# Kernel optimization log

Hardware: AMD Instinct MI355X
Metric: run time of the kernel (lower is better)

## Reference

```python
import jax, jax.numpy as jnp
import numpy as np

N = 100000      # nodes
E = 1600000     # edges (avg degree 16)
DIM = 128
HEADS = 8
HEAD_DIM = DIM // HEADS


def setup_inputs() -> dict:
    key = jax.random.key(0)
    k = jax.random.split(key, 6)
    stdv = 1.0 / np.sqrt(HEAD_DIM)  # init scale from reset_parameters
    x = jax.random.normal(k[0], (N, DIM), dtype=jnp.float32)
    edge_index = jax.random.randint(k[1], (2, E), 0, N, dtype=jnp.int32)
    W = jax.random.uniform(k[2], (DIM, DIM), jnp.float32, -stdv, stdv)
    b_proj = jnp.zeros((DIM,), jnp.float32)
    att_src = jax.random.uniform(k[3], (1, HEADS, HEAD_DIM), jnp.float32, -stdv, stdv)
    att_dst = jax.random.uniform(k[4], (1, HEADS, HEAD_DIM), jnp.float32, -stdv, stdv)
    bias = jnp.zeros((DIM,), jnp.float32)
    return {"x": x, "edge_index": edge_index, "W": W, "b_proj": b_proj,
            "att_src": att_src, "att_dst": att_dst, "bias": bias}


def reference(x, edge_index, W, b_proj, att_src, att_dst, bias):
    n = x.shape[0]
    # project, split heads: [N, H, Hd]
    xh = (x @ W.T + b_proj).reshape(n, HEADS, HEAD_DIM)
    # add_remaining_self_loops (random edges assumed loop-free)
    loops = jnp.arange(n, dtype=edge_index.dtype)
    src = jnp.concatenate([edge_index[0], loops])  # x_j index
    dst = jnp.concatenate([edge_index[1], loops])  # aggregation index
    # per-node attention logits [N, H]
    a_src = jnp.einsum('nhd,hd->nh', xh, att_src[0])
    a_dst = jnp.einsum('nhd,hd->nh', xh, att_dst[0])
    # per-edge score [Etot, H]
    alpha = jax.nn.leaky_relu(a_src[src] + a_dst[dst], negative_slope=0.2)
    # segment softmax over edges grouped by destination (self loops => no empty segments)
    mx = jax.ops.segment_max(alpha, dst, num_segments=n)
    ex = jnp.exp(alpha - mx[dst])
    denom = jax.ops.segment_sum(ex, dst, num_segments=n)
    alpha = ex / denom[dst]
    # message = alpha * x_j, scatter-add to destination
    msg = alpha[:, :, None] * xh[src]                      # [Etot, H, Hd]
    out = jax.ops.segment_sum(msg, dst, num_segments=n)    # [N, H, Hd]
    return out.reshape(n, DIM) + bias
```

## Files before the change

kernel.cpp:

```cpp
#include <hip/hip_runtime.h>
#include <hip/hip_bf16.h>

typedef __hip_bfloat16 bf16;
typedef __hip_bfloat162 bf162;
typedef __attribute__((ext_vector_type(8))) short short8;
typedef __attribute__((ext_vector_type(4))) float f32x4;

#define NN 100000
#define NE 1600000
#define ETOT (NE + NN)
#define DIM 128
#define HEADS 8

#define BSH 9
#define NBUK ((NN + 511) >> BSH)
#define EPB 2048
#define B1 ((ETOT + EPB - 1) / EPB)
#define MAXPER 40

__device__ __forceinline__ float lrelu(float v) { return v > 0.f ? v : 0.2f * v; }

__device__ __forceinline__ float load1(const void* p, int i, int isbf) {
    return isbf ? __bfloat162float(((const bf16*)p)[i]) : ((const float*)p)[i];
}
__device__ __forceinline__ float2 load2(const void* p, size_t pairIdx, int isbf) {
    if (isbf) return __bfloat1622float2(((const bf162*)p)[pairIdx]);
    return ((const float2*)p)[pairIdx];
}
__device__ __forceinline__ short f2bf(float f) {
    bf16 h = __float2bfloat16(f);
    return *reinterpret_cast<short*>(&h);
}

__global__ __launch_bounds__(256) void aug_kernel(
    const void* __restrict__ W, const void* __restrict__ bproj,
    const void* __restrict__ atts, const void* __restrict__ attd,
    int* __restrict__ flag, bf16* __restrict__ waug, float* __restrict__ wc)
{
    __shared__ bf16 Wl[128 * 128];
    __shared__ float av[256];
    __shared__ float red[256];
    const int tid = threadIdx.x;

    {
        const bf16* wb = (const bf16*)W;
        float m = 0.f;
        for (int i = tid; i < 8192; i += 256) {
            float v = fabsf(__bfloat162float(wb[i]));
            if (!(v < 1e30f)) v = 1e30f;
            m = fmaxf(m, v);
        }
        red[tid] = m;
        __syncthreads();
        for (int s = 128; s > 0; s >>= 1) {
            if (tid < s) red[tid] = fmaxf(red[tid], red[tid + s]);
            __syncthreads();
        }
    }
    const int isbf = (red[0] < 1.0f) ? 1 : 0;
    if (tid == 0) *flag = isbf;

    for (int i = tid; i < 2048; i += 256) {
        short8 v;
        if (isbf) {
            v = ((const short8*)W)[i];
        } else {
            const float* wp = (const float*)W + (size_t)i * 8;
            #pragma unroll
            for (int j = 0; j < 8; ++j) v[j] = f2bf(wp[j]);
        }
        ((short8*)Wl)[i] = v;
    }
    av[tid & 255] = (tid < 128) ? load1(atts, tid, isbf)
                                : load1(attd, tid - 128, isbf);
    __syncthreads();

    #pragma unroll
    for (int it = 0; it < 8; ++it) {
        const int o = tid + it * 256;
        const int row = o >> 7, col = o & 127;
        const int h = row & 7;
        const int ao = (row < 8) ? 0 : 128;
        float s = 0.f;
        #pragma unroll
        for (int t = 0; t < 16; ++t)
            s += av[ao + h * 16 + t] * __bfloat162float(Wl[(h * 16 + t) * 128 + col]);
        waug[o] = __float2bfloat16(s);
    }
    if (tid < 16) {
        const int h = tid & 7;
        const int ao = (tid < 8) ? 0 : 128;
        float s = 0.f;
        #pragma unroll
        for (int t = 0; t < 16; ++t)
            s += load1(bproj, h * 16 + t, isbf) * av[ao + h * 16 + t];
        wc[tid] = s;
    }
}

__global__ __launch_bounds__(256) void proj_mfma_kernel(
    const void* __restrict__ x, const void* __restrict__ W,
    const void* __restrict__ bproj, const bf16* __restrict__ waug,
    const float* __restrict__ wc, const int* __restrict__ flag,
    bf16* __restrict__ xh, float* __restrict__ asrc, float* __restrict__ adst)
{
    __shared__ short8 Wf[2304];
    __shared__ float bsh[DIM], csh[16];

    const int isbf = *flag;
    const int tid = threadIdx.x;

    for (int c = tid; c < 2048; c += 256) {
        int j = c >> 4, kc = c & 15;
        int kb = kc >> 2, quad = kc & 3;
        int lane = quad * 16 + (j & 15);
        int jt = j >> 4;
        short8 v;
        if (isbf) {
            v = ((const short8*)W)[c];
        } else {
            const float* wp = (const float*)W + (size_t)j * DIM + kc * 8;
            #pragma unroll
            for (int i = 0; i < 8; ++i) v[i] = f2bf(wp[i]);
        }
        Wf[(jt * 4 + kb) * 64 + lane] = v;
    }
    {
        int c = tid;
        if (c < 256) {
            int j2 = c >> 4, kc = c & 15;
            int kb = kc >> 2, quad = kc & 3;
            Wf[(32 + kb) * 64 + quad * 16 + j2] = ((const short8*)waug)[c];
        }
    }
    if (tid < DIM) bsh[tid] = load1(bproj, tid, isbf);
    if (tid < 16)  csh[tid] = wc[tid];
    __syncthreads();

    const int w = tid >> 6;
    const int l = tid & 63;
    const int quad = l >> 4, mr = l & 15;
    const int n0 = blockIdx.x * 64 + w * 16;
    const int nArd = min(n0 + mr, NN - 1);

    short8 afr[4];
    if (isbf) {
        const short8* xp = (const short8*)x + (size_t)nArd * 16;
        #pragma unroll
        for (int kb = 0; kb < 4; ++kb) afr[kb] = xp[kb * 4 + quad];
    } else {
        const float* xp = (const float*)x + (size_t)nArd * DIM;
        #pragma unroll
        for (int kb = 0; kb < 4; ++kb) {
            const float* cp = xp + kb * 32 + quad * 8;
            float4 c0 = *(const float4*)cp;
            float4 c1 = *(const float4*)(cp + 4);
            short8 v;
            v[0] = f2bf(c0.x); v[1] = f2bf(c0.y); v[2] = f2bf(c0.z); v[3] = f2bf(c0.w);
            v[4] = f2bf(c1.x); v[5] = f2bf(c1.y); v[6] = f2bf(c1.z); v[7] = f2bf(c1.w);
            afr[kb] = v;
        }
    }

    f32x4 accs[8];
    #pragma unroll
    for (int jt = 0; jt < 8; ++jt) {
        f32x4 acc = {0.f, 0.f, 0.f, 0.f};
        #pragma unroll
        for (int kb = 0; kb < 4; ++kb) {
            short8 b = Wf[(jt * 4 + kb) * 64 + l];
            acc = __builtin_amdgcn_mfma_f32_16x16x32_bf16(afr[kb], b, acc, 0, 0, 0);
        }
        accs[jt] = acc;
    }
    f32x4 acca = {0.f, 0.f, 0.f, 0.f};
    #pragma unroll
    for (int kb = 0; kb < 4; ++kb) {
        short8 b = Wf[(32 + kb) * 64 + l];
        acca = __builtin_amdgcn_mfma_f32_16x16x32_bf16(afr[kb], b, acca, 0, 0, 0);
    }

    __syncthreads();

    bf16* sw = ((bf16*)Wf) + w * (16 * 136);
    #pragma unroll
    for (int jt = 0; jt < 8; ++jt) {
        const int jj = jt * 16 + mr;
        const float bv = bsh[jj];
        #pragma unroll
        for (int r = 0; r < 4; ++r)
            sw[(quad * 4 + r) * 136 + jj] = __float2bfloat16(accs[jt][r] + bv);
    }
    #pragma unroll
    for (int g = 0; g < 4; ++g) {
        const int row = g * 4 + (l >> 4);
        const int n = n0 + row;
        if (n < NN)
            *((short8*)(xh + (size_t)n * DIM) + (l & 15)) =
                *(const short8*)(sw + row * 136 + (l & 15) * 8);
    }

    {
        const float cst = csh[mr];
        #pragma unroll
        for (int r = 0; r < 4; ++r) {
            const int n = n0 + quad * 4 + r;
            if (n < NN) {
                float v = acca[r] + cst;
                if (mr < 8) asrc[n * HEADS + mr] = v;
                else        adst[n * HEADS + (mr - 8)] = v;
            }
        }
    }
}

__global__ __launch_bounds__(256) void csr_count_kernel(const int* __restrict__ ei,
                                                        int* __restrict__ cntmat)
{
    __shared__ int cnt[NBUK];
    const int t = threadIdx.x, b = blockIdx.x;
    for (int i = t; i < NBUK; i += 256) cnt[i] = 0;
    __syncthreads();
    const int base = b * EPB;
    #pragma unroll
    for (int it = 0; it < EPB / 1024; ++it) {
        const int e = base + it * 1024 + t * 4;
        if (e < ETOT) {
            int4 d4;
            if (e < NE) {
                d4 = *(const int4*)(ei + NE + e);
            } else {
                d4.x = e - NE; d4.y = d4.x + 1; d4.z = d4.x + 2; d4.w = d4.x + 3;
            }
            atomicAdd(&cnt[d4.x >> BSH], 1);
            atomicAdd(&cnt[d4.y >> BSH], 1);
            atomicAdd(&cnt[d4.z >> BSH], 1);
            atomicAdd(&cnt[d4.w >> BSH], 1);
        }
    }
    __syncthreads();
    for (int k = t; k < NBUK; k += 256) cntmat[k * B1 + b] = cnt[k];
}

__global__ __launch_bounds__(256) void csr_colscan_kernel(const int* __restrict__ cntmat,
                                                          int* __restrict__ cntpre,
                                                          int* __restrict__ btot)
{
    const int k = blockIdx.x, t = threadIdx.x;
    int v[4];
    int s = 0;
    #pragma unroll
    for (int j = 0; j < 4; ++j) {
        const int c = t * 4 + j;
        v[j] = (c < B1) ? cntmat[k * B1 + c] : 0;
        s += v[j];
    }
    const int l = t & 63, w = t >> 6;
    int inc = s;
    #pragma unroll
    for (int off = 1; off < 64; off <<= 1) {
        int u = __shfl_up(inc, off);
        if (l >= off) inc += u;
    }
    __shared__ int wt[4];
    if (l == 63) wt[w] = inc;
    __syncthreads();
    int add = 0;
    #pragma unroll
    for (int i = 0; i < 4; ++i) if (i < w) add += wt[i];
    int run = add + inc - s;
    #pragma unroll
    for (int j = 0; j < 4; ++j) {
        const int c = t * 4 + j;
        if (c < B1) cntpre[k * B1 + c] = run;
        run += v[j];
    }
    if (t == 255) btot[k] = add + inc;
}

__global__ __launch_bounds__(256) void csr_base_kernel(const int* __restrict__ btot,
                                                       int* __restrict__ bbase,
                                                       int* __restrict__ rowstart)
{
    const int t = threadIdx.x;
    const int v = (t < NBUK) ? btot[t] : 0;
    const int l = t & 63, w = t >> 6;
    int inc = v;
    #pragma unroll
    for (int off = 1; off < 64; off <<= 1) {
        int u = __shfl_up(inc, off);
        if (l >= off) inc += u;
    }
    __shared__ int wt[4];
    if (l == 63) wt[w] = inc;
    __syncthreads();
    int add = 0;
    #pragma unroll
    for (int i = 0; i < 4; ++i) if (i < w) add += wt[i];
    if (t < NBUK) bbase[t] = add + inc - v;
    if (t == 0) rowstart[NN] = ETOT;
}

__global__ __launch_bounds__(256) void csr_scatter_kernel(const int* __restrict__ ei,
                                                          const int* __restrict__ cntpre,
                                                          const int* __restrict__ bbase,
                                                          int* __restrict__ esrc)
{
    __shared__ int cur[NBUK];
    const int t = threadIdx.x, b = blockIdx.x;
    for (int k = t; k < NBUK; k += 256) cur[k] = bbase[k] + cntpre[k * B1 + b];
    __syncthreads();
    const int base = b * EPB;
    #pragma unroll
    for (int it = 0; it < EPB / 1024; ++it) {
        const int e = base + it * 1024 + t * 4;
        if (e < ETOT) {
            int4 d4, s4;
            if (e < NE) {
                s4 = *(const int4*)(ei + e);
                d4 = *(const int4*)(ei + NE + e);
            } else {
                s4.x = e - NE; s4.y = s4.x + 1; s4.z = s4.x + 2; s4.w = s4.x + 3;
                d4 = s4;
            }
            const int p0 = atomicAdd(&cur[d4.x >> BSH], 1);
            const int p1 = atomicAdd(&cur[d4.y >> BSH], 1);
            const int p2 = atomicAdd(&cur[d4.z >> BSH], 1);
            const int p3 = atomicAdd(&cur[d4.w >> BSH], 1);
            esrc[p0] = s4.x | ((d4.x & 511) << 17);
            esrc[p1] = s4.y | ((d4.y & 511) << 17);
            esrc[p2] = s4.z | ((d4.z & 511) << 17);
            esrc[p3] = s4.w | ((d4.w & 511) << 17);
        }
    }
}

__global__ __launch_bounds__(256) void csr_bucket_kernel(const int* __restrict__ bbase,
                                                         int* __restrict__ esrc,
                                                         int* __restrict__ rowstart)
{
    __shared__ int hist[512];
    __shared__ int pre[512];
    __shared__ int wt[4];
    const int k = blockIdx.x, t = threadIdx.x;
    const int start = bbase[k];
    const int end = (k == NBUK - 1) ? ETOT : bbase[k + 1];

    hist[t] = 0;
    hist[t + 256] = 0;
    __syncthreads();

    int v[MAXPER];
    #pragma unroll
    for (int j = 0; j < MAXPER; ++j) {
        const int idx = start + j * 256 + t;
        v[j] = (idx < end) ? esrc[idx] : -1;
    }
    #pragma unroll
    for (int j = 0; j < MAXPER; ++j)
        if (v[j] >= 0) atomicAdd(&hist[(v[j] >> 17) & 511], 1);
    __syncthreads();

    const int h0 = hist[2 * t], h1 = hist[2 * t + 1];
    const int pv = h0 + h1;
    const int l = t & 63, w = t >> 6;
    int inc = pv;
    #pragma unroll
    for (int off = 1; off < 64; off <<= 1) {
        int u = __shfl_up(inc, off);
        if (l >= off) inc += u;
    }
    if (l == 63) wt[w] = inc;
    __syncthreads();
    int add = 0;
    #pragma unroll
    for (int i = 0; i < 4; ++i) if (i < w) add += wt[i];
    const int ex = add + inc - pv;
    pre[2 * t] = ex;
    pre[2 * t + 1] = ex + h0;

    const int d0 = (k << BSH) + 2 * t;
    if (d0 < NN)     rowstart[d0]     = start + ex;
    if (d0 + 1 < NN) rowstart[d0 + 1] = start + ex + h0;
    __syncthreads();

    #pragma unroll
    for (int j = 0; j < MAXPER; ++j) {
        if (v[j] >= 0) {
            const int pos = atomicAdd(&pre[(v[j] >> 17) & 511], 1);
            esrc[start + pos] = v[j] & 0x1FFFF;
        }
    }
}

__global__ __launch_bounds__(256) void gather_kernel(
    const int* __restrict__ rowstart, const int* __restrict__ esrc,
    const float* __restrict__ asrc, const float* __restrict__ adst,
    const bf16* __restrict__ xh, const void* __restrict__ bias,
    const int* __restrict__ flag, void* __restrict__ out)
{
    const int d = blockIdx.x * 4 + (threadIdx.x >> 6);
    if (d >= NN) return;
    const int l = threadIdx.x & 63;
    const int h = l >> 3;
    const int isbf = *flag;

    const float ad = adst[d * HEADS + h];
    const int r0 = rowstart[d], r1 = rowstart[d + 1];
    const bf162* __restrict__ xrow = (const bf162*)xh;
    float a0 = 0.f, a1 = 0.f, ds = 0.f;

    int p = r0;
    for (; p + 8 <= r1; p += 8) {
        int s[8];
        #pragma unroll
        for (int j = 0; j < 8; ++j) s[j] = esrc[p + j];
        float v[8];
        #pragma unroll
        for (int j = 0; j < 8; ++j) v[j] = asrc[(unsigned)s[j] * HEADS + h];
        float2 xv[8];
        #pragma unroll
        for (int j = 0; j < 8; ++j)
            xv[j] = __bfloat1622float2(xrow[(unsigned)s[j] * 64u + (unsigned)l]);
        #pragma unroll
        for (int j = 0; j < 8; ++j) {
            float wj = __expf(lrelu(v[j] + ad));
            a0 += wj * xv[j].x;
            a1 += wj * xv[j].y;
            ds += wj;
        }
    }
    for (; p + 4 <= r1; p += 4) {
        int s0 = esrc[p + 0], s1 = esrc[p + 1], s2 = esrc[p + 2], s3 = esrc[p + 3];
        float v0 = asrc[(unsigned)s0 * HEADS + h];
        float v1 = asrc[(unsigned)s1 * HEADS + h];
        float v2 = asrc[(unsigned)s2 * HEADS + h];
        float v3 = asrc[(unsigned)s3 * HEADS + h];
        float2 x0 = __bfloat1622float2(xrow[(unsigned)s0 * 64u + (unsigned)l]);
        float2 x1 = __bfloat1622float2(xrow[(unsigned)s1 * 64u + (unsigned)l]);
        float2 x2 = __bfloat1622float2(xrow[(unsigned)s2 * 64u + (unsigned)l]);
        float2 x3 = __bfloat1622float2(xrow[(unsigned)s3 * 64u + (unsigned)l]);
        float w0 = __expf(lrelu(v0 + ad));
        float w1 = __expf(lrelu(v1 + ad));
        float w2 = __expf(lrelu(v2 + ad));
        float w3 = __expf(lrelu(v3 + ad));
        a0 += w0 * x0.x + w1 * x1.x + w2 * x2.x + w3 * x3.x;
        a1 += w0 * x0.y + w1 * x1.y + w2 * x2.y + w3 * x3.y;
        ds += (w0 + w1) + (w2 + w3);
    }
    for (; p < r1; ++p) {
        int s = esrc[p];
        float w = __expf(lrelu(asrc[(unsigned)s * HEADS + h] + ad));
        float2 xf = __bfloat1622float2(xrow[(unsigned)s * 64u + (unsigned)l]);
        a0 += w * xf.x;
        a1 += w * xf.y;
        ds += w;
    }

    float inv = 1.f / ds;
    float2 bf = load2(bias, l, isbf);
    float o0 = a0 * inv + bf.x;
    float o1 = a1 * inv + bf.y;
    if (isbf) {
        bf162 o;
        o.x = __float2bfloat16(o0);
        o.y = __float2bfloat16(o1);
        ((bf162*)out)[(size_t)d * 64 + l] = o;
    } else {
        ((float2*)out)[(size_t)d * 64 + l] = make_float2(o0, o1);
    }
}

extern "C" void kernel_launch(void* const* d_in, const int* in_sizes, int n_in,
                              void* d_out, int out_size, void* d_ws, size_t ws_size,
                              hipStream_t stream)
{
    const void* x     = d_in[0];
    const int*  ei    = (const int*)d_in[1];
    const void* W     = d_in[2];
    const void* bproj = d_in[3];
    const void* atts  = d_in[4];
    const void* attd  = d_in[5];
    const void* bias  = d_in[6];

    char* p = (char*)d_ws;
    int*    flag     = (int*)p;    p += 16;
    bf16*   xh       = (bf16*)p;   p += (size_t)NN * DIM * sizeof(bf16);
    float*  asrc     = (float*)p;  p += (size_t)NN * HEADS * sizeof(float);
    float*  adst     = (float*)p;  p += (size_t)NN * HEADS * sizeof(float);
    int*    rowstart = (int*)p;    p += (size_t)(NN + 1) * sizeof(int) + 12;
    int*    esrc     = (int*)p;    p += (size_t)ETOT * sizeof(int);
    int*    cntmat   = (int*)p;    p += (size_t)NBUK * B1 * sizeof(int);
    int*    cntpre   = (int*)p;    p += (size_t)NBUK * B1 * sizeof(int);
    int*    btot     = (int*)p;    p += ((NBUK + 3) & ~3) * sizeof(int);
    int*    bbase    = (int*)p;    p += ((NBUK + 3) & ~3) * sizeof(int);
    bf16*   waug     = (bf16*)p;   p += 16 * 128 * sizeof(bf16);
    float*  wc       = (float*)p;  p += 16 * sizeof(float);

    aug_kernel<<<1, 256, 0, stream>>>(W, bproj, atts, attd, flag, waug, wc);
    proj_mfma_kernel<<<(NN + 63) / 64, 256, 0, stream>>>(x, W, bproj, waug, wc,
                                                         flag, xh, asrc, adst);
    csr_count_kernel<<<B1, 256, 0, stream>>>(ei, cntmat);
    csr_colscan_kernel<<<NBUK, 256, 0, stream>>>(cntmat, cntpre, btot);
    csr_base_kernel<<<1, 256, 0, stream>>>(btot, bbase, rowstart);
    csr_scatter_kernel<<<B1, 256, 0, stream>>>(ei, cntpre, bbase, esrc);
    csr_bucket_kernel<<<NBUK, 256, 0, stream>>>(bbase, esrc, rowstart);
    gather_kernel<<<(NN + 3) / 4, 256, 0, stream>>>(rowstart, esrc, asrc, adst,
                                                    xh, bias, flag, d_out);
}
```

Baseline: 280.0 us.

## Fold attention-weight prep into projection and fuse CSR build into cooperative kernel

Removes the single-block aug_kernel by having every projection block recompute the attention-augmented weight rows and constants in shared memory. The five CSR-construction kernels are merged into one cooperative kernel that uses grid-wide syncs between the count, column-scan, base-scan, scatter and bucket-sort phases. The old multi-kernel path is kept as a fallback if the cooperative launch fails. This targets launch overhead and inter-kernel gaps, at the cost of redundant per-block weight computation, grid-sync latency, and a grid of about 830 blocks that must all be co-resident.

```diff
diff --git a/kernel.cpp b/kernel.cpp
--- a/kernel.cpp
+++ b/kernel.cpp
@@ -1,5 +1,8 @@
 #include <hip/hip_runtime.h>
 #include <hip/hip_bf16.h>
+#include <hip/hip_cooperative_groups.h>
+
+namespace cg = cooperative_groups;
 
 typedef __hip_bfloat16 bf16;
 typedef __hip_bfloat162 bf162;
@@ -32,14 +35,17 @@
     return *reinterpret_cast<short*>(&h);
 }
 
-__global__ __launch_bounds__(256) void aug_kernel(
-    const void* __restrict__ W, const void* __restrict__ bproj,
-    const void* __restrict__ atts, const void* __restrict__ attd,
-    int* __restrict__ flag, bf16* __restrict__ waug, float* __restrict__ wc)
-{
-    __shared__ bf16 Wl[128 * 128];
+__global__ __launch_bounds__(256) void proj_mfma_kernel(
+    const void* __restrict__ x, const void* __restrict__ W,
+    const void* __restrict__ bproj, const void* __restrict__ atts,
+    const void* __restrict__ attd, int* __restrict__ flag,
+    bf16* __restrict__ xh, float* __restrict__ asrc, float* __restrict__ adst)
+{
+    __shared__ short8 Wf[2304];
+    __shared__ float bsh[DIM], csh[16];
     __shared__ float av[256];
     __shared__ float red[256];
+
     const int tid = threadIdx.x;
 
     {
@@ -58,57 +64,7 @@
         }
     }
     const int isbf = (red[0] < 1.0f) ? 1 : 0;
-    if (tid == 0) *flag = isbf;
-
-    for (int i = tid; i < 2048; i += 256) {
-        short8 v;
-        if (isbf) {
-            v = ((const short8*)W)[i];
-        } else {
-            const float* wp = (const float*)W + (size_t)i * 8;
-            #pragma unroll
-            for (int j = 0; j < 8; ++j) v[j] = f2bf(wp[j]);
-        }
-        ((short8*)Wl)[i] = v;
-    }
-    av[tid & 255] = (tid < 128) ? load1(atts, tid, isbf)
-                                : load1(attd, tid - 128, isbf);
-    __syncthreads();
-
-    #pragma unroll
-    for (int it = 0; it < 8; ++it) {
-        const int o = tid + it * 256;
-        const int row = o >> 7, col = o & 127;
-        const int h = row & 7;
-        const int ao = (row < 8) ? 0 : 128;
-        float s = 0.f;
-        #pragma unroll
-        for (int t = 0; t < 16; ++t)
-            s += av[ao + h * 16 + t] * __bfloat162float(Wl[(h * 16 + t) * 128 + col]);
-        waug[o] = __float2bfloat16(s);
-    }
-    if (tid < 16) {
-        const int h = tid & 7;
-        const int ao = (tid < 8) ? 0 : 128;
-        float s = 0.f;
-        #pragma unroll
-        for (int t = 0; t < 16; ++t)
-            s += load1(bproj, h * 16 + t, isbf) * av[ao + h * 16 + t];
-        wc[tid] = s;
-    }
-}
-
-__global__ __launch_bounds__(256) void proj_mfma_kernel(
-    const void* __restrict__ x, const void* __restrict__ W,
-    const void* __restrict__ bproj, const bf16* __restrict__ waug,
-    const float* __restrict__ wc, const int* __restrict__ flag,
-    bf16* __restrict__ xh, float* __restrict__ asrc, float* __restrict__ adst)
-{
-    __shared__ short8 Wf[2304];
-    __shared__ float bsh[DIM], csh[16];
-
-    const int isbf = *flag;
-    const int tid = threadIdx.x;
+    if (blockIdx.x == 0 && tid == 0) *flag = isbf;
 
     for (int c = tid; c < 2048; c += 256) {
         int j = c >> 4, kc = c & 15;
@@ -125,16 +81,40 @@
         }
         Wf[(jt * 4 + kb) * 64 + lane] = v;
     }
+    if (tid < DIM) bsh[tid] = load1(bproj, tid, isbf);
+    av[tid] = (tid < 128) ? load1(atts, tid, isbf)
+                          : load1(attd, tid - 128, isbf);
+    __syncthreads();
+
     {
-        int c = tid;
-        if (c < 256) {
-            int j2 = c >> 4, kc = c & 15;
-            int kb = kc >> 2, quad = kc & 3;
-            Wf[(32 + kb) * 64 + quad * 16 + j2] = ((const short8*)waug)[c];
-        }
-    }
-    if (tid < DIM) bsh[tid] = load1(bproj, tid, isbf);
-    if (tid < 16)  csh[tid] = wc[tid];
+        const int kb = tid >> 6;
+        const int lane = tid & 63;
+        const int quad = (tid >> 4) & 3;
+        const int j2 = tid & 15;
+        const int h = j2 & 7;
+        const int ao = (j2 < 8) ? 0 : 128;
+        short8 vv;
+        #pragma unroll
+        for (int c = 0; c < 8; ++c) {
+            float s = 0.f;
+            #pragma unroll
+            for (int t = 0; t < 16; ++t) {
+                const bf16* wp = (const bf16*)&Wf[(h * 4 + kb) * 64 + quad * 16 + t];
+                s += av[ao + h * 16 + t] * __bfloat162float(wp[c]);
+            }
+            vv[c] = f2bf(s);
+        }
+        Wf[(32 + kb) * 64 + lane] = vv;
+    }
+    if (tid < 16) {
+        const int h = tid & 7;
+        const int ao = (tid < 8) ? 0 : 128;
+        float s = 0.f;
+        #pragma unroll
+        for (int t = 0; t < 16; ++t)
+            s += bsh[h * 16 + t] * av[ao + h * 16 + t];
+        csh[tid] = s;
+    }
     __syncthreads();
 
     const int w = tid >> 6;
@@ -209,6 +189,175 @@
                 float v = acca[r] + cst;
                 if (mr < 8) asrc[n * HEADS + mr] = v;
                 else        adst[n * HEADS + (mr - 8)] = v;
+            }
+        }
+    }
+}
+
+__global__ __launch_bounds__(256, 4) void csr_coop_kernel(
+    const int* __restrict__ ei, int* __restrict__ cntmat,
+    int* __restrict__ cntpre, int* __restrict__ btot,
+    int* __restrict__ bbase, int* __restrict__ esrc,
+    int* __restrict__ rowstart)
+{
+    cg::grid_group grid = cg::this_grid();
+    __shared__ int sh[1028];
+    const int t = threadIdx.x, b = blockIdx.x;
+
+    for (int i = t; i < NBUK; i += 256) sh[i] = 0;
+    __syncthreads();
+    {
+        const int base = b * EPB;
+        #pragma unroll
+        for (int it = 0; it < EPB / 1024; ++it) {
+            const int e = base + it * 1024 + t * 4;
+            if (e < ETOT) {
+                int4 d4;
+                if (e < NE) {
+                    d4 = *(const int4*)(ei + NE + e);
+                } else {
+                    d4.x = e - NE; d4.y = d4.x + 1; d4.z = d4.x + 2; d4.w = d4.x + 3;
+                }
+                atomicAdd(&sh[d4.x >> BSH], 1);
+                atomicAdd(&sh[d4.y >> BSH], 1);
+                atomicAdd(&sh[d4.z >> BSH], 1);
+                atomicAdd(&sh[d4.w >> BSH], 1);
+            }
+        }
+    }
+    __syncthreads();
+    for (int k = t; k < NBUK; k += 256) cntmat[k * B1 + b] = sh[k];
+    grid.sync();
+
+    if (b < NBUK) {
+        const int k = b;
+        int v[4];
+        int s = 0;
+        #pragma unroll
+        for (int j = 0; j < 4; ++j) {
+            const int c = t * 4 + j;
+            v[j] = (c < B1) ? cntmat[k * B1 + c] : 0;
+            s += v[j];
+        }
+        const int l = t & 63, w = t >> 6;
+        int inc = s;
+        #pragma unroll
+        for (int off = 1; off < 64; off <<= 1) {
+            int u = __shfl_up(inc, off);
+            if (l >= off) inc += u;
+        }
+        if (l == 63) sh[1024 + w] = inc;
+        __syncthreads();
+        int add = 0;
+        #pragma unroll
+        for (int i = 0; i < 4; ++i) if (i < w) add += sh[1024 + i];
+        int run = add + inc - s;
+        #pragma unroll
+        for (int j = 0; j < 4; ++j) {
+            const int c = t * 4 + j;
+            if (c < B1) cntpre[k * B1 + c] = run;
+            run += v[j];
+        }
+        if (t == 255) btot[k] = add + inc;
+    }
+    grid.sync();
+
+    if (b == 0) {
+        const int v = (t < NBUK) ? btot[t] : 0;
+        const int l = t & 63, w = t >> 6;
+        int inc = v;
+        #pragma unroll
+        for (int off = 1; off < 64; off <<= 1) {
+            int u = __shfl_up(inc, off);
+            if (l >= off) inc += u;
+        }
+        if (l == 63) sh[1024 + w] = inc;
+        __syncthreads();
+        int add = 0;
+        #pragma unroll
+        for (int i = 0; i < 4; ++i) if (i < w) add += sh[1024 + i];
+        if (t < NBUK) bbase[t] = add + inc - v;
+        if (t == 0) rowstart[NN] = ETOT;
+    }
+    grid.sync();
+
+    for (int k = t; k < NBUK; k += 256) sh[k] = bbase[k] + cntpre[k * B1 + b];
+    __syncthreads();
+    {
+        const int base = b * EPB;
+        #pragma unroll
+        for (int it = 0; it < EPB / 1024; ++it) {
+            const int e = base + it * 1024 + t * 4;
+            if (e < ETOT) {
+                int4 d4, s4;
+                if (e < NE) {
+                    s4 = *(const int4*)(ei + e);
+                    d4 = *(const int4*)(ei + NE + e);
+                } else {
+                    s4.x = e - NE; s4.y = s4.x + 1; s4.z = s4.x + 2; s4.w = s4.x + 3;
+                    d4 = s4;
+                }
+                const int p0 = atomicAdd(&sh[d4.x >> BSH], 1);
+                const int p1 = atomicAdd(&sh[d4.y >> BSH], 1);
+                const int p2 = atomicAdd(&sh[d4.z >> BSH], 1);
+                const int p3 = atomicAdd(&sh[d4.w >> BSH], 1);
+                esrc[p0] = s4.x | ((d4.x & 511) << 17);
+                esrc[p1] = s4.y | ((d4.y & 511) << 17);
+                esrc[p2] = s4.z | ((d4.z & 511) << 17);
+                esrc[p3] = s4.w | ((d4.w & 511) << 17);
+            }
+        }
+    }
+    grid.sync();
+
+    if (b < NBUK) {
+        const int k = b;
+        const int start = bbase[k];
+        const int end = (k == NBUK - 1) ? ETOT : bbase[k + 1];
+
+        sh[t] = 0;
+        sh[t + 256] = 0;
+        __syncthreads();
+
+        int v[MAXPER];
+        #pragma unroll
+        for (int j = 0; j < MAXPER; ++j) {
+            const int idx = start + j * 256 + t;
+            v[j] = (idx < end) ? esrc[idx] : -1;
+        }
+        #pragma unroll
+        for (int j = 0; j < MAXPER; ++j)
+            if (v[j] >= 0) atomicAdd(&sh[(v[j] >> 17) & 511], 1);
+        __syncthreads();
+
+        const int h0 = sh[2 * t], h1 = sh[2 * t + 1];
+        const int pv = h0 + h1;
+        const int l = t & 63, w = t >> 6;
+        int inc = pv;
+        #pragma unroll
+        for (int off = 1; off < 64; off <<= 1) {
+            int u = __shfl_up(inc, off);
+            if (l >= off) inc += u;
+        }
+        if (l == 63) sh[1024 + w] = inc;
+        __syncthreads();
+        int add = 0;
+        #pragma unroll
+        for (int i = 0; i < 4; ++i) if (i < w) add += sh[1024 + i];
+        const int ex = add + inc - pv;
+        sh[512 + 2 * t] = ex;
+        sh[512 + 2 * t + 1] = ex + h0;
+
+        const int d0 = (k << BSH) + 2 * t;
+        if (d0 < NN)     rowstart[d0]     = start + ex;
+        if (d0 + 1 < NN) rowstart[d0 + 1] = start + ex + h0;
+        __syncthreads();
+
+        #pragma unroll
+        for (int j = 0; j < MAXPER; ++j) {
+            if (v[j] >= 0) {
+                const int pos = atomicAdd(&sh[512 + ((v[j] >> 17) & 511)], 1);
+                esrc[start + pos] = v[j] & 0x1FFFF;
             }
         }
     }
@@ -494,17 +643,25 @@
     int*    cntpre   = (int*)p;    p += (size_t)NBUK * B1 * sizeof(int);
     int*    btot     = (int*)p;    p += ((NBUK + 3) & ~3) * sizeof(int);
     int*    bbase    = (int*)p;    p += ((NBUK + 3) & ~3) * sizeof(int);
-    bf16*   waug     = (bf16*)p;   p += 16 * 128 * sizeof(bf16);
-    float*  wc       = (float*)p;  p += 16 * sizeof(float);
-
-    aug_kernel<<<1, 256, 0, stream>>>(W, bproj, atts, attd, flag, waug, wc);
-    proj_mfma_kernel<<<(NN + 63) / 64, 256, 0, stream>>>(x, W, bproj, waug, wc,
+
+    proj_mfma_kernel<<<(NN + 63) / 64, 256, 0, stream>>>(x, W, bproj, atts, attd,
                                                          flag, xh, asrc, adst);
-    csr_count_kernel<<<B1, 256, 0, stream>>>(ei, cntmat);
-    csr_colscan_kernel<<<NBUK, 256, 0, stream>>>(cntmat, cntpre, btot);
-    csr_base_kernel<<<1, 256, 0, stream>>>(btot, bbase, rowstart);
-    csr_scatter_kernel<<<B1, 256, 0, stream>>>(ei, cntpre, bbase, esrc);
-    csr_bucket_kernel<<<NBUK, 256, 0, stream>>>(bbase, esrc, rowstart);
+
+    {
+        void* cargs[] = {(void*)&ei, (void*)&cntmat, (void*)&cntpre, (void*)&btot,
+                         (void*)&bbase, (void*)&esrc, (void*)&rowstart};
+        hipError_t cerr = hipLaunchCooperativeKernel(
+            reinterpret_cast<void*>(csr_coop_kernel), dim3(B1), dim3(256),
+            cargs, 0, stream);
+        if (cerr != hipSuccess) {
+            csr_count_kernel<<<B1, 256, 0, stream>>>(ei, cntmat);
+            csr_colscan_kernel<<<NBUK, 256, 0, stream>>>(cntmat, cntpre, btot);
+            csr_base_kernel<<<1, 256, 0, stream>>>(btot, bbase, rowstart);
+            csr_scatter_kernel<<<B1, 256, 0, stream>>>(ei, cntpre, bbase, esrc);
+            csr_bucket_kernel<<<NBUK, 256, 0, stream>>>(bbase, esrc, rowstart);
+        }
+    }
+
     gather_kernel<<<(NN + 3) / 4, 256, 0, stream>>>(rowstart, esrc, asrc, adst,
                                                     xh, bias, flag, d_out);
 }
```

Result: slower. 674.3 us (+140.8%).

## Fuse CSR counting into projection launch and fold bucket-base scan into consumers

Applied to the files above, without the earlier changes.

Adds the CSR destination-count blocks as extra blocks of the projection kernel, so both independent jobs run in one launch and can overlap. Removes the single-block base-scan kernel by having every scatter and bucket block recompute the small prefix scan over bucket totals in shared memory. This saves two kernel launches and their serialization gaps, at the cost of redundant per-block scan work and shared-memory reuse of the projection's weight buffer.

```diff
diff --git a/kernel.cpp b/kernel.cpp
--- a/kernel.cpp
+++ b/kernel.cpp
@@ -17,6 +17,7 @@
 #define EPB 2048
 #define B1 ((ETOT + EPB - 1) / EPB)
 #define MAXPER 40
+#define PROJ_BLKS ((NN + 63) / 64)
 
 __device__ __forceinline__ float lrelu(float v) { return v > 0.f ? v : 0.2f * v; }
 
@@ -98,17 +99,46 @@
     }
 }
 
-__global__ __launch_bounds__(256) void proj_mfma_kernel(
+__global__ __launch_bounds__(256) void projcount_kernel(
     const void* __restrict__ x, const void* __restrict__ W,
     const void* __restrict__ bproj, const bf16* __restrict__ waug,
     const float* __restrict__ wc, const int* __restrict__ flag,
-    bf16* __restrict__ xh, float* __restrict__ asrc, float* __restrict__ adst)
+    bf16* __restrict__ xh, float* __restrict__ asrc, float* __restrict__ adst,
+    const int* __restrict__ ei, int* __restrict__ cntmat)
 {
     __shared__ short8 Wf[2304];
     __shared__ float bsh[DIM], csh[16];
 
+    const int tid = threadIdx.x;
+
+    if (blockIdx.x >= PROJ_BLKS) {
+        const int b = blockIdx.x - PROJ_BLKS;
+        int* cnt = (int*)Wf;
+        for (int i = tid; i < NBUK; i += 256) cnt[i] = 0;
+        __syncthreads();
+        const int base = b * EPB;
+        #pragma unroll
+        for (int it = 0; it < EPB / 1024; ++it) {
+            const int e = base + it * 1024 + tid * 4;
+            if (e < ETOT) {
+                int4 d4;
+                if (e < NE) {
+                    d4 = *(const int4*)(ei + NE + e);
+                } else {
+                    d4.x = e - NE; d4.y = d4.x + 1; d4.z = d4.x + 2; d4.w = d4.x + 3;
+                }
+                atomicAdd(&cnt[d4.x >> BSH], 1);
+                atomicAdd(&cnt[d4.y >> BSH], 1);
+                atomicAdd(&cnt[d4.z >> BSH], 1);
+                atomicAdd(&cnt[d4.w >> BSH], 1);
+            }
+        }
+        __syncthreads();
+        for (int k = tid; k < NBUK; k += 256) cntmat[k * B1 + b] = cnt[k];
+        return;
+    }
+
     const int isbf = *flag;
-    const int tid = threadIdx.x;
 
     for (int c = tid; c < 2048; c += 256) {
         int j = c >> 4, kc = c & 15;
@@ -214,34 +244,6 @@
     }
 }
 
-__global__ __launch_bounds__(256) void csr_count_kernel(const int* __restrict__ ei,
-                                                        int* __restrict__ cntmat)
-{
-    __shared__ int cnt[NBUK];
-    const int t = threadIdx.x, b = blockIdx.x;
-    for (int i = t; i < NBUK; i += 256) cnt[i] = 0;
-    __syncthreads();
-    const int base = b * EPB;
-    #pragma unroll
-    for (int it = 0; it < EPB / 1024; ++it) {
-        const int e = base + it * 1024 + t * 4;
-        if (e < ETOT) {
-            int4 d4;
-            if (e < NE) {
-                d4 = *(const int4*)(ei + NE + e);
-            } else {
-                d4.x = e - NE; d4.y = d4.x + 1; d4.z = d4.x + 2; d4.w = d4.x + 3;
-            }
-            atomicAdd(&cnt[d4.x >> BSH], 1);
-            atomicAdd(&cnt[d4.y >> BSH], 1);
-            atomicAdd(&cnt[d4.z >> BSH], 1);
-            atomicAdd(&cnt[d4.w >> BSH], 1);
-        }
-    }
-    __syncthreads();
-    for (int k = t; k < NBUK; k += 256) cntmat[k * B1 + b] = cnt[k];
-}
-
 __global__ __launch_bounds__(256) void csr_colscan_kernel(const int* __restrict__ cntmat,
                                                           int* __restrict__ cntpre,
                                                           int* __restrict__ btot)
@@ -278,9 +280,8 @@
     if (t == 255) btot[k] = add + inc;
 }
 
-__global__ __launch_bounds__(256) void csr_base_kernel(const int* __restrict__ btot,
-                                                       int* __restrict__ bbase,
-                                                       int* __restrict__ rowstart)
+__device__ __forceinline__ void scan_btot(const int* __restrict__ btot,
+                                          int* __restrict__ bb, int* __restrict__ wt4)
 {
     const int t = threadIdx.x;
     const int v = (t < NBUK) ? btot[t] : 0;
@@ -291,25 +292,29 @@
         int u = __shfl_up(inc, off);
         if (l >= off) inc += u;
     }
-    __shared__ int wt[4];
-    if (l == 63) wt[w] = inc;
+    if (l == 63) wt4[w] = inc;
     __syncthreads();
     int add = 0;
     #pragma unroll
-    for (int i = 0; i < 4; ++i) if (i < w) add += wt[i];
-    if (t < NBUK) bbase[t] = add + inc - v;
-    if (t == 0) rowstart[NN] = ETOT;
+    for (int i = 0; i < 4; ++i) if (i < w) add += wt4[i];
+    if (t < NBUK) bb[t] = add + inc - v;
+    __syncthreads();
 }
 
 __global__ __launch_bounds__(256) void csr_scatter_kernel(const int* __restrict__ ei,
                                                           const int* __restrict__ cntpre,
-                                                          const int* __restrict__ bbase,
+                                                          const int* __restrict__ btot,
                                                           int* __restrict__ esrc)
 {
     __shared__ int cur[NBUK];
+    __shared__ int bb[NBUK];
+    __shared__ int wt4[4];
     const int t = threadIdx.x, b = blockIdx.x;
-    for (int k = t; k < NBUK; k += 256) cur[k] = bbase[k] + cntpre[k * B1 + b];
-    __syncthreads();
+
+    scan_btot(btot, bb, wt4);
+    for (int k = t; k < NBUK; k += 256) cur[k] = bb[k] + cntpre[k * B1 + b];
+    __syncthreads();
+
     const int base = b * EPB;
     #pragma unroll
     for (int it = 0; it < EPB / 1024; ++it) {
@@ -335,16 +340,20 @@
     }
 }
 
-__global__ __launch_bounds__(256) void csr_bucket_kernel(const int* __restrict__ bbase,
+__global__ __launch_bounds__(256) void csr_bucket_kernel(const int* __restrict__ btot,
                                                          int* __restrict__ esrc,
                                                          int* __restrict__ rowstart)
 {
     __shared__ int hist[512];
     __shared__ int pre[512];
-    __shared__ int wt[4];
+    __shared__ int bb[NBUK];
+    __shared__ int wt4[4];
     const int k = blockIdx.x, t = threadIdx.x;
-    const int start = bbase[k];
-    const int end = (k == NBUK - 1) ? ETOT : bbase[k + 1];
+
+    scan_btot(btot, bb, wt4);
+    const int start = bb[k];
+    const int end = start + btot[k];
+    if (k == 0 && t == 0) rowstart[NN] = ETOT;
 
     hist[t] = 0;
     hist[t + 256] = 0;
@@ -370,11 +379,11 @@
         int u = __shfl_up(inc, off);
         if (l >= off) inc += u;
     }
-    if (l == 63) wt[w] = inc;
+    if (l == 63) wt4[w] = inc;
     __syncthreads();
     int add = 0;
     #pragma unroll
-    for (int i = 0; i < 4; ++i) if (i < w) add += wt[i];
+    for (int i = 0; i < 4; ++i) if (i < w) add += wt4[i];
     const int ex = add + inc - pv;
     pre[2 * t] = ex;
     pre[2 * t + 1] = ex + h0;
@@ -493,18 +502,16 @@
     int*    cntmat   = (int*)p;    p += (size_t)NBUK * B1 * sizeof(int);
     int*    cntpre   = (int*)p;    p += (size_t)NBUK * B1 * sizeof(int);
     int*    btot     = (int*)p;    p += ((NBUK + 3) & ~3) * sizeof(int);
-    int*    bbase    = (int*)p;    p += ((NBUK + 3) & ~3) * sizeof(int);
     bf16*   waug     = (bf16*)p;   p += 16 * 128 * sizeof(bf16);
     float*  wc       = (float*)p;  p += 16 * sizeof(float);
 
     aug_kernel<<<1, 256, 0, stream>>>(W, bproj, atts, attd, flag, waug, wc);
-    proj_mfma_kernel<<<(NN + 63) / 64, 256, 0, stream>>>(x, W, bproj, waug, wc,
-                                                         flag, xh, asrc, adst);
-    csr_count_kernel<<<B1, 256, 0, stream>>>(ei, cntmat);
+    projcount_kernel<<<PROJ_BLKS + B1, 256, 0, stream>>>(x, W, bproj, waug, wc,
+                                                         flag, xh, asrc, adst,
+                                                         ei, cntmat);
     csr_colscan_kernel<<<NBUK, 256, 0, stream>>>(cntmat, cntpre, btot);
-    csr_base_kernel<<<1, 256, 0, stream>>>(btot, bbase, rowstart);
-    csr_scatter_kernel<<<B1, 256, 0, stream>>>(ei, cntpre, bbase, esrc);
-    csr_bucket_kernel<<<NBUK, 256, 0, stream>>>(bbase, esrc, rowstart);
+    csr_scatter_kernel<<<B1, 256, 0, stream>>>(ei, cntpre, btot, esrc);
+    csr_bucket_kernel<<<NBUK, 256, 0, stream>>>(btot, esrc, rowstart);
     gather_kernel<<<(NN + 3) / 4, 256, 0, stream>>>(rowstart, esrc, asrc, adst,
                                                     xh, bias, flag, d_out);
 }
```

Measured after the change: 274.9 us. About the same (-1.8%).
